# Kernel optimization log

Hardware: AMD Instinct MI355X
Metric: run time of the kernel (lower is better)

## Reference

```python
import jax, jax.numpy as jnp
import numpy as np
import math

B, N, K, H = 128, 39, 10, 256
RATIO = 0.8
K1 = math.ceil(RATIO * N)    # 32
K2 = math.ceil(RATIO * K1)   # 26
K3 = math.ceil(RATIO * K2)   # 21


def _edge_conv(x_flat, nb, n, w, b):
    # DynamicEdgeConv: per-graph kNN on features (self included, as torch_cluster.knn),
    # message = relu(Linear([x_i, x_j - x_i])), max aggregation over the K neighbors.
    f = x_flat.shape[-1]
    x = x_flat.reshape(nb, n, f)
    sq = jnp.sum(x * x, axis=-1)                                   # [nb,n]
    d = sq[:, :, None] + sq[:, None, :] - 2.0 * jnp.einsum('bif,bjf->bij', x, x)
    _, idx = jax.lax.top_k(-d, K)                                  # [nb,n,K] nearest
    xj = x[jnp.arange(nb)[:, None, None], idx]                     # [nb,n,K,f]
    xi = x[:, :, None, :]
    msg = jnp.concatenate([jnp.broadcast_to(xi, xj.shape), xj - xi], axis=-1)
    h = jax.nn.relu(msg @ w + b)
    return jnp.max(h, axis=2).reshape(nb * n, -1)


def _gcn_score(x_flat, adj, w, b):
    # GCNConv(in,1) with self-loops + symmetric normalization (SAGPool score layer)
    nb, n, _ = adj.shape
    x = x_flat.reshape(nb, n, -1)
    a = adj + jnp.eye(n, dtype=adj.dtype)
    dinv = jax.lax.rsqrt(jnp.sum(a, axis=-1))
    an = a * dinv[:, :, None] * dinv[:, None, :]
    s = jnp.einsum('bij,bjf->bif', an, x @ w) + b
    return s[..., 0]                                               # [nb,n]


def _sag_pool(x_flat, adj, k, w, b):
    # SAGPool: GCN score, per-graph top-k, gate kept nodes by tanh(score), filter adj.
    nb, n, _ = adj.shape
    score = _gcn_score(x_flat, adj, w, b)
    top, loc = jax.lax.top_k(score, k)                             # [nb,k]
    bi = jnp.arange(nb)[:, None]
    x = x_flat.reshape(nb, n, -1)
    xp = x[bi, loc] * jnp.tanh(top)[..., None]
    adj_p = adj[jnp.arange(nb)[:, None, None], loc[:, :, None], loc[:, None, :]]
    perm = (bi * n + loc).reshape(-1)                              # flat node ids
    return xp.reshape(nb * k, -1), adj_p, perm


def _bn(x, g, b, eps=1e-5):
    m = jnp.mean(x, axis=0)
    v = jnp.var(x, axis=0)
    return (x - m) * jax.lax.rsqrt(v + eps) * g + b


def _readout(x_flat, nb, k):
    x = x_flat.reshape(nb, k, -1)
    return jnp.concatenate([jnp.max(x, axis=1), jnp.mean(x, axis=1)], axis=1)


def reference(x, adj, w_mlp1, b_mlp1, w_mlp2, b_mlp2, w_mlp3, b_mlp3, w_mlp6, b_mlp6,
              bn1_g, bn1_b, bn2_g, bn2_b, bn3_g, bn3_b,
              p1_w, p1_b, p2_w, p2_b, p3_w, p3_b,
              lin1_w, lin1_b, lin2_w, lin2_b, lin3_w, lin3_b,
              lin4_w, lin4_b, lin5_w, lin5_b, lin6_w, lin6_b):
    relu = jax.nn.relu
    deg_gt = jnp.sum(adj, axis=-1).reshape(B * N)                  # degree(edge_index[0])

    def decoder(xf):
        d = jnp.tanh(_edge_conv(xf, B, N, w_mlp3, b_mlp3))         # conv4
        d = jnp.tanh(_edge_conv(d, B, N, w_mlp2, b_mlp2))          # conv5
        return _edge_conv(d, B, N, w_mlp6, b_mlp6)                 # conv6

    def degree_head(xf):
        h = relu(xf @ lin4_w + lin4_b)
        h = relu(h @ lin5_w + lin5_b)
        return relu(h @ lin6_w + lin6_b)

    # ---- level 1 ----
    h1 = relu(_bn(_edge_conv(x.reshape(B * N, N), B, N, w_mlp1, b_mlp1), bn1_g, bn1_b))
    xp1, adj1, perm1 = _sag_pool(h1, adj, K1, p1_w, p1_b)
    x_out1 = jnp.zeros_like(h1).at[perm1].set(xp1)
    x_dec1 = decoder(x_out1)
    x_degree = degree_head(x_out1)   # source reuses this tensor for levels 2/3 preds
    gt1, pred1 = deg_gt[perm1], x_degree[perm1]
    r1 = _readout(xp1, B, K1)

    # ---- level 2 ----
    h2 = relu(_bn(_edge_conv(xp1, B, K1, w_mlp2, b_mlp2), bn2_g, bn2_b))
    xp2, adj2, perm2 = _sag_pool(h2, adj1, K2, p2_w, p2_b)
    inner2 = jnp.zeros_like(h2).at[perm2].set(xp2)
    x_out2 = jnp.zeros_like(h1).at[perm1].set(inner2)
    x_dec2 = decoder(x_out2)
    gt2, pred2 = deg_gt[perm2], x_degree[perm2]
    r2 = _readout(xp2, B, K2)

    # ---- level 3 ----
    h3 = relu(_bn(_edge_conv(xp2, B, K2, w_mlp3, b_mlp3), bn3_g, bn3_b))
    xp3, adj3, perm3 = _sag_pool(h3, adj2, K3, p3_w, p3_b)
    inner3 = jnp.zeros_like(h3).at[perm3].set(xp3)
    x_out3 = jnp.zeros_like(h1).at[perm2].set(inner3)  # faithful: source uses perm_2 here
    x_dec3 = decoder(x_out3)
    gt3, pred3 = deg_gt[perm3], x_degree[perm3]
    r3 = _readout(xp3, B, K3)

    z = r1 + r2 + r3
    z = relu(z @ lin1_w + lin1_b)
    z = relu(z @ lin2_w + lin2_b)
    probs = jax.nn.softmax(z @ lin3_w + lin3_b, axis=1)
    return (probs, x_dec1, x_dec2, x_dec3, gt1, pred1, gt2, pred2, gt3, pred3)


def setup_inputs() -> dict:
    key = jax.random.key(0)
    ks = jax.random.split(key, 32)
    rn = lambda i, shape: jax.random.normal(ks[i], shape, dtype=jnp.float32) * 0.05
    x = jax.random.normal(ks[0], (B, N, N), dtype=jnp.float32)
    adj = (jax.random.uniform(ks[1], (B, N, N)) < 0.2).astype(jnp.float32)
    adj = adj * (1.0 - jnp.eye(N, dtype=jnp.float32))
    return dict(
        x=x, adj=adj,
        w_mlp1=rn(2, (2 * N, H)), b_mlp1=rn(3, (H,)),
        w_mlp2=rn(4, (2 * H, H)), b_mlp2=rn(5, (H,)),
        w_mlp3=rn(6, (2 * H, H)), b_mlp3=rn(7, (H,)),
        w_mlp6=rn(8, (2 * H, N)), b_mlp6=rn(9, (N,)),
        bn1_g=jnp.ones((H,), jnp.float32), bn1_b=jnp.zeros((H,), jnp.float32),
        bn2_g=jnp.ones((H,), jnp.float32), bn2_b=jnp.zeros((H,), jnp.float32),
        bn3_g=jnp.ones((H,), jnp.float32), bn3_b=jnp.zeros((H,), jnp.float32),
        p1_w=rn(10, (H, 1)), p1_b=rn(11, (1,)),
        p2_w=rn(12, (H, 1)), p2_b=rn(13, (1,)),
        p3_w=rn(14, (H, 1)), p3_b=rn(15, (1,)),
        lin1_w=rn(16, (2 * H, H)), lin1_b=rn(17, (H,)),
        lin2_w=rn(18, (H, H // 2)), lin2_b=rn(19, (H // 2,)),
        lin3_w=rn(20, (H // 2, 2)), lin3_b=rn(21, (2,)),
        lin4_w=rn(22, (H, H)), lin4_b=rn(23, (H,)),
        lin5_w=rn(24, (H, H // 2)), lin5_b=rn(25, (H // 2,)),
        lin6_w=rn(26, (H // 2, 1)), lin6_b=rn(27, (1,)))
```

## Files before the change

### kernel.cpp

```cpp
#include <hip/hip_runtime.h>
#include <cmath>

#define B_   128
#define N_   39
#define KNN_ 10
#define H_   256
#define K1_  32
#define K2_  26
#define K3_  21

static inline int cdiv(int a, int b) { return (a + b - 1) / b; }

typedef __attribute__((ext_vector_type(8))) short short8;
typedef __attribute__((ext_vector_type(4))) short short4v;
typedef __attribute__((ext_vector_type(4))) float floatx4;

__device__ inline short f2b(float f) {
  unsigned u = __float_as_uint(f);
  u += 0x7fff + ((u >> 16) & 1);
  return (short)(u >> 16);
}
__device__ inline float b2f(short h) {
  return __uint_as_float(((unsigned)(unsigned short)h) << 16);
}
__device__ inline void f2b3(float v, short& h, short& m, short& l) {
  h = f2b(v);
  float r1 = v - b2f(h);
  m = f2b(r1);
  l = f2b(r1 - b2f(m));
}

__device__ __forceinline__ void gl_lds16(const short* g, short* l) {
  __builtin_amdgcn_global_load_lds(
      (const __attribute__((address_space(1))) unsigned int*)g,
      (__attribute__((address_space(3))) unsigned int*)l, 16, 0, 0);
}

__global__ void prep_kernel(
    const float* __restrict__ w1, const float* __restrict__ w2,
    const float* __restrict__ w3, const float* __restrict__ w6,
    const float* __restrict__ l4, const float* __restrict__ l5,
    const float* __restrict__ x, const float* __restrict__ adj,
    short* __restrict__ wt1h, short* __restrict__ wt1m, short* __restrict__ wt1l,
    short* __restrict__ wt2h, short* __restrict__ wt2m, short* __restrict__ wt2l,
    short* __restrict__ wt3h, short* __restrict__ wt3m, short* __restrict__ wt3l,
    short* __restrict__ wt6h, short* __restrict__ wt6m,
    short* __restrict__ l4h, short* __restrict__ l4m,
    short* __restrict__ l5h, short* __restrict__ l5m,
    short* __restrict__ xsph, short* __restrict__ xspm, short* __restrict__ xspl,
    float* __restrict__ deg, short* __restrict__ zbase, double* __restrict__ bnsum) {
  int blk = blockIdx.x;
  int task, base;
  if      (blk < 128)  { task = 0; base = 0; }
  else if (blk < 640)  { task = 1; base = 128; }
  else if (blk < 1152) { task = 2; base = 640; }
  else if (blk < 1230) { task = 3; base = 1152; }
  else if (blk < 1486) { task = 4; base = 1230; }
  else if (blk < 1614) { task = 5; base = 1486; }
  else if (blk < 2862) { task = 6; base = 1614; }
  else if (blk < 2882) { task = 7; base = 2862; }
  else if (blk < 6626) { task = 8; base = 2882; }
  else                 { task = 9; base = 6626; }
  int t = (blk - base) * 256 + threadIdx.x;
  if (task == 0) {
    if (t >= 512 * 64) return;
    int nn = t >> 6, k = t & 63;
    float v = 0.f;
    if (k < 39) v = (nn < 256) ? w1[k * 256 + nn] - w1[(39 + k) * 256 + nn]
                               : w1[(39 + k) * 256 + (nn - 256)];
    short h, m, l; f2b3(v, h, m, l);
    wt1h[t] = h; wt1m[t] = m; wt1l[t] = l;
  } else if (task == 1) {
    if (t >= 512 * 256) return;
    int nn = t >> 8, k = t & 255;
    float v = (nn < 256) ? w2[k * 256 + nn] - w2[(256 + k) * 256 + nn]
                         : w2[(256 + k) * 256 + (nn - 256)];
    short h, m, l; f2b3(v, h, m, l);
    wt2h[t] = h; wt2m[t] = m; wt2l[t] = l;
  } else if (task == 2) {
    if (t >= 512 * 256) return;
    int nn = t >> 8, k = t & 255;
    float v = (nn < 256) ? w3[k * 256 + nn] - w3[(256 + k) * 256 + nn]
                         : w3[(256 + k) * 256 + (nn - 256)];
    short h, m, l; f2b3(v, h, m, l);
    wt3h[t] = h; wt3m[t] = m; wt3l[t] = l;
  } else if (task == 3) {
    if (t >= 78 * 256) return;
    int nn = t >> 8, k = t & 255;
    float v = (nn < 39) ? w6[k * 39 + nn] - w6[(256 + k) * 39 + nn]
                        : w6[(256 + k) * 39 + (nn - 39)];
    short h, m, l; f2b3(v, h, m, l);
    wt6h[t] = h; wt6m[t] = m;
  } else if (task == 4) {
    if (t >= 256 * 256) return;
    int nn = t >> 8, k = t & 255;
    short h, m, l; f2b3(l4[k * 256 + nn], h, m, l);
    l4h[t] = h; l4m[t] = m;
  } else if (task == 5) {
    if (t >= 128 * 256) return;
    int nn = t >> 8, k = t & 255;
    short h, m, l; f2b3(l5[k * 128 + nn], h, m, l);
    l5h[t] = h; l5m[t] = m;
  } else if (task == 6) {
    if (t >= 4992 * 64) return;
    int r = t >> 6, k = t & 63;
    float v = (k < 39) ? x[r * 39 + k] : 0.f;
    short h, m, l; f2b3(v, h, m, l);
    xsph[t] = h; xspm[t] = m; xspl[t] = l;
  } else if (task == 7) {
    if (t >= B_ * N_) return;
    const float* row = adj + (size_t)t * N_;
    float s = 0.f;
    for (int j = 0; j < N_; ++j) s += row[j];
    deg[t] = s;
  } else if (task == 8) {
    if (t >= 958464) return;
    short8 zz = {};
    *(short8*)&zbase[(size_t)t * 8] = zz;
  } else {
    if (t >= 256) return;
    for (int j = 0; j < 6; ++j) bnsum[t + j * 256] = 0.0;
  }
}

__global__ __launch_bounds__(512) void knn_gemm_kernel(
    const short* __restrict__ kxh, const short* __restrict__ kxm, const short* __restrict__ kxl,
    int knt, int kKs, int kn, int kF32, int* __restrict__ idx, int knnB,
    const short* __restrict__ Ah, const short* __restrict__ Am, const short* __restrict__ Al,
    int gnt, int gK,
    const short* __restrict__ Wh, const short* __restrict__ Wm, const short* __restrict__ Wl,
    float* __restrict__ C0, int gM, int gN, int gyB,
    size_t Astride, size_t Cstride) {
  extern __shared__ char smem[];
  int tid = threadIdx.x;
  int wave = tid >> 6, lane = tid & 63;
  int lm = lane & 15, lk = (lane >> 4) * 8;
  if ((int)blockIdx.x < knnB) {
    short* sh_h = (short*)smem;
    short* sh_m = sh_h + 48 * 40;
    short* sh_l = sh_m + 48 * 40;
    float* Gs   = (float*)(sh_l + 48 * 40);
    float* diag = Gs + 48 * 49;
    int b = blockIdx.x;
    int nt = (kn + 15) >> 4;
    int tasks = nt * nt;
    floatx4 acc[2] = {};
    int stage_elems = 384 * knt;
    for (int k0 = 0; k0 < kF32; k0 += 32) {
      for (int e = tid; e < stage_elems; e += 512) {
        int a = e / 384, rem = e - a * 384;
        int r = rem >> 3, c4 = (rem & 7) * 4;
        const short* src = (a == 0) ? kxh : (a == 1) ? kxm : kxl;
        short* dst = (a == 0) ? sh_h : (a == 1) ? sh_m : sh_l;
        *(short4v*)&dst[r * 40 + c4] =
            *(const short4v*)&src[((size_t)(b * kn + r)) * kKs + k0 + c4];
      }
      __syncthreads();
#pragma unroll
      for (int ai = 0; ai < 2; ++ai) {
        int t = wave + ai * 8;
        if (t < tasks) {
          int ti = t / nt, tj = t - ti * nt;
          int ra = (ti * 16 + lm) * 40 + lk;
          int rb = (tj * 16 + lm) * 40 + lk;
          short8 ah = *(const short8*)&sh_h[ra];
          short8 am = *(const short8*)&sh_m[ra];
          short8 bh = *(const short8*)&sh_h[rb];
          short8 bm = *(const short8*)&sh_m[rb];
          floatx4 a = acc[ai];
          a = __builtin_amdgcn_mfma_f32_16x16x32_bf16(ah, bh, a, 0, 0, 0);
          a = __builtin_amdgcn_mfma_f32_16x16x32_bf16(ah, bm, a, 0, 0, 0);
          a = __builtin_amdgcn_mfma_f32_16x16x32_bf16(am, bh, a, 0, 0, 0);
          if (knt == 3) {
            short8 al = *(const short8*)&sh_l[ra];
            short8 bl = *(const short8*)&sh_l[rb];
            a = __builtin_amdgcn_mfma_f32_16x16x32_bf16(ah, bl, a, 0, 0, 0);
            a = __builtin_amdgcn_mfma_f32_16x16x32_bf16(al, bh, a, 0, 0, 0);
            a = __builtin_amdgcn_mfma_f32_16x16x32_bf16(am, bm, a, 0, 0, 0);
          }
          acc[ai] = a;
        }
      }
      __syncthreads();
    }
#pragma unroll
    for (int ai = 0; ai < 2; ++ai) {
      int t = wave + ai * 8;
      if (t < tasks) {
        int ti = t / nt, tj = t - ti * nt;
        int col = tj * 16 + lm;
        int rbase = ti * 16 + (lane >> 4) * 4;
#pragma unroll
        for (int r = 0; r < 4; ++r) Gs[(rbase + r) * 49 + col] = acc[ai][r];
      }
    }
    __syncthreads();
    if (tid < 48) diag[tid] = (tid < kn) ? Gs[tid * 49 + tid] : INFINITY;
    __syncthreads();
    for (int row = wave; row < kn; row += 8) {
      float gii = diag[row];
      float dj = (lane < kn) ? (gii + diag[lane] - 2.f * Gs[row * 49 + lane]) : INFINITY;
      int rank = 0;
      for (int j = 0; j < kn; ++j) {
        float djp = gii + diag[j] - 2.f * Gs[row * 49 + j];
        rank += (djp < dj || (djp == dj && j < lane)) ? 1 : 0;
      }
      if (lane < kn && rank < KNN_)
        idx[(size_t)(b * kn + row) * KNN_ + rank] = lane;
    }
  } else {
    short* AshL = (short*)smem;
    short* AsmL = AshL + 4096;
    short* AslL = AsmL + 4096;
    short* BshL = (short*)smem + gnt * 4096;
    short* BsmL = BshL + 4096;
    short* BslL = BsmL + 4096;
    int gb = blockIdx.x - knnB;
    int gxB = (gN + 127) >> 7;
    int nb = (int)gridDim.x - knnB;
    int xcd = gb & 7, j = gb >> 3;
    int q8 = nb >> 3, r8 = nb & 7;
    int work = (xcd < r8 ? xcd * (q8 + 1) : r8 * (q8 + 1) + (xcd - r8) * q8) + j;
    int gx = work % gxB;
    int rest = work / gxB;
    int gy = rest % gyB;
    int gz = rest / gyB;
    const short* A_h = Ah + (size_t)gz * Astride;
    const short* A_m = Am ? Am + (size_t)gz * Astride : nullptr;
    const short* A_l = Al ? Al + (size_t)gz * Astride : nullptr;
    float* C = C0 + (size_t)gz * Cstride;
    int row0 = gy * 128, col0 = gx * 128;
    int wm = wave & 1, wn = wave >> 1;
    int srow = tid >> 2;
    int scs = ((tid & 3) ^ ((srow >> 1) & 3)) << 3;
    size_t gArow = (size_t)(row0 + srow) * gK;
    size_t gBrow = (size_t)(col0 + srow) * gK;
    short* ldsA = AshL + tid * 8;
    short* ldsAm = AsmL + tid * 8;
    short* ldsAl = AslL + tid * 8;
    short* ldsB = BshL + tid * 8;
    short* ldsBm = BsmL + tid * 8;
    short* ldsBl = BslL + tid * 8;
    floatx4 acc[4][2] = {};
    for (int k0 = 0; k0 < gK; k0 += 32) {
      gl_lds16(A_h + gArow + k0 + scs, ldsA);
      gl_lds16(A_m + gArow + k0 + scs, ldsAm);
      if (gnt == 3) gl_lds16(A_l + gArow + k0 + scs, ldsAl);
      gl_lds16(Wh + gBrow + k0 + scs, ldsB);
      gl_lds16(Wm + gBrow + k0 + scs, ldsBm);
      if (gnt == 3) gl_lds16(Wl + gBrow + k0 + scs, ldsBl);
      __syncthreads();
      short8 afh[4], afm[4], afl[4];
#pragma unroll
      for (int mi = 0; mi < 4; ++mi) {
        int rr = wm * 64 + mi * 16 + lm;
        int ro = rr * 32 + (((lane >> 4) ^ ((rr >> 1) & 3)) << 3);
        afh[mi] = *(const short8*)&AshL[ro];
        afm[mi] = *(const short8*)&AsmL[ro];
        if (gnt == 3) afl[mi] = *(const short8*)&AslL[ro];
      }
#pragma unroll
      for (int ni = 0; ni < 2; ++ni) {
        int rb = wn * 32 + ni * 16 + lm;
        int ro = rb * 32 + (((lane >> 4) ^ ((rb >> 1) & 3)) << 3);
        short8 bfh = *(const short8*)&BshL[ro];
        short8 bfm = *(const short8*)&BsmL[ro];
#pragma unroll
        for (int mi = 0; mi < 4; ++mi) {
          floatx4 a = acc[mi][ni];
          a = __builtin_amdgcn_mfma_f32_16x16x32_bf16(afh[mi], bfh, a, 0, 0, 0);
          a = __builtin_amdgcn_mfma_f32_16x16x32_bf16(afh[mi], bfm, a, 0, 0, 0);
          a = __builtin_amdgcn_mfma_f32_16x16x32_bf16(afm[mi], bfh, a, 0, 0, 0);
          if (gnt == 3) {
            short8 bfl = *(const short8*)&BslL[ro];
            a = __builtin_amdgcn_mfma_f32_16x16x32_bf16(afh[mi], bfl, a, 0, 0, 0);
            a = __builtin_amdgcn_mfma_f32_16x16x32_bf16(afl[mi], bfh, a, 0, 0, 0);
            a = __builtin_amdgcn_mfma_f32_16x16x32_bf16(afm[mi], bfm, a, 0, 0, 0);
          }
          acc[mi][ni] = a;
        }
      }
      __syncthreads();
    }
    int lr = (lane >> 4) * 4;
#pragma unroll
    for (int mi = 0; mi < 4; ++mi)
#pragma unroll
      for (int ni = 0; ni < 2; ++ni) {
        int colg = col0 + wn * 32 + ni * 16 + lm;
        if (colg >= gN) continue;
#pragma unroll
        for (int r = 0; r < 4; ++r) {
          int rowg = row0 + wm * 64 + mi * 16 + lr + r;
          C[(size_t)rowg * gN + colg] = acc[mi][ni][r];
        }
      }
  }
}

__global__ __launch_bounds__(256) void degree_head_kernel(
    const short* __restrict__ Xh, const short* __restrict__ Xm,
    const short* __restrict__ W4h, const short* __restrict__ W4m, const float* __restrict__ b4,
    const short* __restrict__ W5h, const short* __restrict__ W5m, const float* __restrict__ b5,
    const float* __restrict__ w6, const float* __restrict__ b6,
    float* __restrict__ xdeg) {
  __shared__ __attribute__((aligned(16))) short Ash[32 * 40];
  __shared__ __attribute__((aligned(16))) short Asm[32 * 40];
  __shared__ __attribute__((aligned(16))) short Bsh[256 * 40];
  __shared__ __attribute__((aligned(16))) short Bsm[256 * 40];
  __shared__ __attribute__((aligned(16))) short H1h[32][264];
  __shared__ __attribute__((aligned(16))) short H1m[32][264];
  __shared__ float rowsum[32];
  int tid = threadIdx.x;
  int wave = tid >> 6, lane = tid & 63;
  int lm = lane & 15, g = lane >> 4, lk = g * 8;
  int row0 = blockIdx.x * 32;

  floatx4 acc[2][4] = {};
  for (int k0 = 0; k0 < 256; k0 += 32) {
    {
      int e = tid;
      int a = e >> 7, rem = e & 127;
      int r = rem >> 2, kc = (rem & 3) * 8;
      const short* src = a ? Xm : Xh;
      short* dst = a ? Asm : Ash;
      *(short8*)&dst[r * 40 + kc] = *(const short8*)&src[(size_t)(row0 + r) * 256 + k0 + kc];
    }
#pragma unroll
    for (int i = 0; i < 8; ++i) {
      int e = tid + i * 256;
      int a = e >> 10, rem = e & 1023;
      int r = rem >> 2, kc = (rem & 3) * 8;
      const short* src = a ? W4m : W4h;
      short* dst = a ? Bsm : Bsh;
      *(short8*)&dst[r * 40 + kc] = *(const short8*)&src[(size_t)r * 256 + k0 + kc];
    }
    __syncthreads();
    short8 afh[2], afm[2];
#pragma unroll
    for (int rt = 0; rt < 2; ++rt) {
      int ro = (rt * 16 + lm) * 40 + lk;
      afh[rt] = *(const short8*)&Ash[ro];
      afm[rt] = *(const short8*)&Asm[ro];
    }
#pragma unroll
    for (int ct = 0; ct < 4; ++ct) {
      int ro = (wave * 64 + ct * 16 + lm) * 40 + lk;
      short8 bfh = *(const short8*)&Bsh[ro];
      short8 bfm = *(const short8*)&Bsm[ro];
#pragma unroll
      for (int rt = 0; rt < 2; ++rt) {
        floatx4 a = acc[rt][ct];
        a = __builtin_amdgcn_mfma_f32_16x16x32_bf16(afh[rt], bfh, a, 0, 0, 0);
        a = __builtin_amdgcn_mfma_f32_16x16x32_bf16(afh[rt], bfm, a, 0, 0, 0);
        a = __builtin_amdgcn_mfma_f32_16x16x32_bf16(afm[rt], bfh, a, 0, 0, 0);
        acc[rt][ct] = a;
      }
    }
    __syncthreads();
  }
#pragma unroll
  for (int rt = 0; rt < 2; ++rt)
#pragma unroll
    for (int ct = 0; ct < 4; ++ct) {
      int col = wave * 64 + ct * 16 + lm;
      float bv = b4[col];
#pragma unroll
      for (int r = 0; r < 4; ++r) {
        int row = rt * 16 + g * 4 + r;
        float v = fmaxf(acc[rt][ct][r] + bv, 0.f);
        short hh = f2b(v);
        H1h[row][col] = hh;
        H1m[row][col] = f2b(v - b2f(hh));
      }
    }
  if (tid < 32) rowsum[tid] = 0.f;
  __syncthreads();

  floatx4 acc2[2][2] = {};
  for (int k0 = 0; k0 < 256; k0 += 32) {
#pragma unroll
    for (int i = 0; i < 4; ++i) {
      int e = tid + i * 256;
      int a = e >> 9, rem = e & 511;
      int r = rem >> 2, kc = (rem & 3) * 8;
      const short* src = a ? W5m : W5h;
      short* dst = a ? Bsm : Bsh;
      *(short8*)&dst[r * 40 + kc] = *(const short8*)&src[(size_t)r * 256 + k0 + kc];
    }
    __syncthreads();
    short8 afh[2], afm[2];
#pragma unroll
    for (int rt = 0; rt < 2; ++rt) {
      afh[rt] = *(const short8*)&H1h[rt * 16 + lm][k0 + lk];
      afm[rt] = *(const short8*)&H1m[rt * 16 + lm][k0 + lk];
    }
#pragma unroll
    for (int ct = 0; ct < 2; ++ct) {
      int ro = (wave * 32 + ct * 16 + lm) * 40 + lk;
      short8 bfh = *(const short8*)&Bsh[ro];
      short8 bfm = *(const short8*)&Bsm[ro];
#pragma unroll
      for (int rt = 0; rt < 2; ++rt) {
        floatx4 a = acc2[rt][ct];
        a = __builtin_amdgcn_mfma_f32_16x16x32_bf16(afh[rt], bfh, a, 0, 0, 0);
        a = __builtin_amdgcn_mfma_f32_16x16x32_bf16(afh[rt], bfm, a, 0, 0, 0);
        a = __builtin_amdgcn_mfma_f32_16x16x32_bf16(afm[rt], bfh, a, 0, 0, 0);
        acc2[rt][ct] = a;
      }
    }
    __syncthreads();
  }
#pragma unroll
  for (int rt = 0; rt < 2; ++rt) {
#pragma unroll
    for (int r = 0; r < 4; ++r) {
      float p = 0.f;
#pragma unroll
      for (int ct = 0; ct < 2; ++ct) {
        int col = wave * 32 + ct * 16 + lm;
        float v = fmaxf(acc2[rt][ct][r] + b5[col], 0.f);
        p += v * w6[col];
      }
#pragma unroll
      for (int off = 1; off < 16; off <<= 1) p += __shfl_xor(p, off, 64);
      if (lm == 0) atomicAdd(&rowsum[rt * 16 + g * 4 + r], p);
    }
  }
  __syncthreads();
  if (tid < 32) xdeg[row0 + tid] = fmaxf(rowsum[tid] + b6[0], 0.f);
}

__global__ void edge_agg_kernel(const float* __restrict__ AB, const float* __restrict__ bias,
                                const int* __restrict__ idx, int n, int Hc, int act,
                                int rows, int per,
                                float* __restrict__ out,
                                short* __restrict__ outh, short* __restrict__ outm,
                                short* __restrict__ outl) {
  int t = blockIdx.x * blockDim.x + threadIdx.x;
  if (t >= rows * Hc) return;
  int r = t / Hc, h = t - r * Hc;
  int d = r / per, rloc = r - d * per;
  int b = rloc / n;
  int s2 = 2 * Hc;
  float av = AB[(size_t)r * s2 + h] + bias[h];
  const int* ir = idx + ((size_t)d * per + rloc) * KNN_;
  int base = d * per + b * n;
  float m = -INFINITY;
  for (int k = 0; k < KNN_; ++k) {
    float v = av + AB[(size_t)(base + ir[k]) * s2 + Hc + h];
    v = fmaxf(v, 0.f);
    m = fmaxf(m, v);
  }
  if (act == 2) m = tanhf(m);
  if (out) out[t] = m;
  if (outh) {
    short hh, mm, ll;
    f2b3(m, hh, mm, ll);
    outh[t] = hh; outm[t] = mm;
    if (outl) outl[t] = ll;
  }
}

__global__ __launch_bounds__(256) void edge_agg4_kernel(
    const float* __restrict__ AB, const float* __restrict__ bias,
    const int* __restrict__ idx, int n, int Hc, int act,
    int rows, int per,
    float* __restrict__ out,
    short* __restrict__ outh, short* __restrict__ outm, short* __restrict__ outl,
    double* __restrict__ colsums) {
  __shared__ double lds_s[4][256];
  __shared__ double lds_s2[4][256];
  int tid = threadIdx.x;
  int hq = tid & 63, rl = tid >> 6;
  int h = hq << 2;
  int s2s = 2 * Hc;
  double cs[4] = {0.0, 0.0, 0.0, 0.0}, cs2[4] = {0.0, 0.0, 0.0, 0.0};
#pragma unroll
  for (int sub = 0; sub < 2; ++sub) {
    int r = blockIdx.x * 8 + rl + sub * 4;
    if (r < rows) {
      int d = r / per, rloc = r - d * per;
      int b = rloc / n;
      float4 av = *(const float4*)&AB[(size_t)r * s2s + h];
      float4 bv = *(const float4*)&bias[h];
      float a0 = av.x + bv.x, a1 = av.y + bv.y, a2 = av.z + bv.z, a3 = av.w + bv.w;
      const int* ir = idx + ((size_t)d * per + rloc) * KNN_;
      int base = d * per + b * n;
      int nb[KNN_];
#pragma unroll
      for (int k = 0; k < KNN_; ++k) nb[k] = base + ir[k];
      float m0 = -INFINITY, m1 = -INFINITY, m2 = -INFINITY, m3 = -INFINITY;
#pragma unroll
      for (int k = 0; k < KNN_; ++k) {
        float4 bb = *(const float4*)&AB[(size_t)nb[k] * s2s + Hc + h];
        m0 = fmaxf(m0, fmaxf(a0 + bb.x, 0.f));
        m1 = fmaxf(m1, fmaxf(a1 + bb.y, 0.f));
        m2 = fmaxf(m2, fmaxf(a2 + bb.z, 0.f));
        m3 = fmaxf(m3, fmaxf(a3 + bb.w, 0.f));
      }
      if (act == 2) { m0 = tanhf(m0); m1 = tanhf(m1); m2 = tanhf(m2); m3 = tanhf(m3); }
      size_t o = (size_t)r * Hc + h;
      if (out) *(float4*)&out[o] = make_float4(m0, m1, m2, m3);
      if (outh) {
        short h0, mm0, l0, h1, mm1, l1, h2, mm2, l2, h3, mm3, l3;
        f2b3(m0, h0, mm0, l0); f2b3(m1, h1, mm1, l1);
        f2b3(m2, h2, mm2, l2); f2b3(m3, h3, mm3, l3);
        short4v vh = {h0, h1, h2, h3};
        short4v vm = {mm0, mm1, mm2, mm3};
        *(short4v*)&outh[o] = vh;
        *(short4v*)&outm[o] = vm;
        if (outl) {
          short4v vl = {l0, l1, l2, l3};
          *(short4v*)&outl[o] = vl;
        }
      }
      if (colsums) {
        double d0 = (double)m0, d1 = (double)m1, d2 = (double)m2, d3 = (double)m3;
        cs[0] += d0; cs2[0] += d0 * d0;
        cs[1] += d1; cs2[1] += d1 * d1;
        cs[2] += d2; cs2[2] += d2 * d2;
        cs[3] += d3; cs2[3] += d3 * d3;
      }
    }
  }
  if (colsums) {
#pragma unroll
    for (int j = 0; j < 4; ++j) {
      lds_s[rl][h + j] = cs[j];
      lds_s2[rl][h + j] = cs2[j];
    }
    __syncthreads();
    int c = tid;
    double ss = ((lds_s[0][c] + lds_s[1][c]) + lds_s[2][c]) + lds_s[3][c];
    double ss2 = ((lds_s2[0][c] + lds_s2[1][c]) + lds_s2[2][c]) + lds_s2[3][c];
    atomicAdd(&colsums[c], ss);
    atomicAdd(&colsums[256 + c], ss2);
  }
}

__global__ __launch_bounds__(1024) void sag_pool_kernel(
    const float* __restrict__ t1,
    const double* __restrict__ colsums, const float* __restrict__ bng,
    const float* __restrict__ bnb, int M,
    const float* __restrict__ pw,
    const float* __restrict__ adj_in, int n, int k,
    const float* __restrict__ pb,
    int* __restrict__ perm, float* __restrict__ adjp,
    const float* __restrict__ deg, const float* __restrict__ xdeg,
    float* __restrict__ gt, float* __restrict__ pred,
    const int* __restrict__ gperm, int gk, float* __restrict__ ggt, float* __restrict__ gpred,
    const int* __restrict__ remap, int accum,
    short* __restrict__ xph, short* __restrict__ xpm, short* __restrict__ xpl,
    short* __restrict__ soh, short* __restrict__ som, float* __restrict__ z,
    const float* __restrict__ W1, const float* __restrict__ b1,
    const float* __restrict__ W2, const float* __restrict__ b2,
    const float* __restrict__ W3, const float* __restrict__ b3,
    float* __restrict__ probs) {
  __shared__ float ys[40], dinv[40], scs[40], tant[40];
  __shared__ int locs[40];
  __shared__ __attribute__((aligned(16))) float t1L[39 * 256];
  __shared__ __attribute__((aligned(16))) float adjL[39 * 39];
  __shared__ __attribute__((aligned(16))) float scshL[512];
  __shared__ __attribute__((aligned(16))) float pmx[4][256];
  __shared__ __attribute__((aligned(16))) float psm[4][256];
  __shared__ __attribute__((aligned(16))) float ca[512];
  __shared__ __attribute__((aligned(16))) float z1s[256];
  __shared__ __attribute__((aligned(16))) float z2s[128];
  __shared__ float lg[2];
  int b = blockIdx.x;
  int i = threadIdx.x;
  int wave = i >> 6, lane = i & 63;
  {
    const float* src = t1 + (size_t)(b * n) * H_;
    int tot = n * H_;
    for (int e = i; e < tot; e += 1024) t1L[e] = src[e];
    const float* asrc = adj_in + (size_t)b * n * n;
    int atot = n * n;
    for (int e = i; e < atot; e += 1024) adjL[e] = asrc[e];
  }
  if (i < 256) {
    double mean = colsums[i] / M;
    double var = colsums[256 + i] / M - mean * mean;
    float rstd = 1.f / sqrtf((float)var + 1e-5f);
    float sc = rstd * bng[i];
    scshL[i] = sc;
    scshL[256 + i] = bnb[i] - (float)mean * sc;
  }
  __syncthreads();
  for (int row = wave; row < n; row += 16) {
    const float* xr = &t1L[row * H_];
    float s = 0.f;
    for (int kk = lane; kk < H_; kk += 64) {
      float v = fmaxf(xr[kk] * scshL[kk] + scshL[H_ + kk], 0.f);
      s += v * pw[kk];
    }
    for (int off = 32; off; off >>= 1) s += __shfl_down(s, off, 64);
    if (lane == 0) ys[row] = s;
  }
  __syncthreads();
  if (i < n) {
    const float* ar = &adjL[i * n];
    float sum = 1.f;
    for (int j = 0; j < n; ++j) sum += ar[j];
    dinv[i] = 1.f / sqrtf(sum);
  }
  __syncthreads();
  if (i < n) {
    const float* ar = &adjL[i * n];
    float acc = 0.f;
    for (int j = 0; j < n; ++j) {
      float a = ar[j] + (i == j ? 1.f : 0.f);
      acc += a * dinv[j] * ys[j];
    }
    scs[i] = dinv[i] * acc + pb[0];
  }
  __syncthreads();
  if (i < n) {
    float si = scs[i];
    int rank = 0;
    for (int j = 0; j < n; ++j) {
      float sj = scs[j];
      rank += (sj > si || (sj == si && j < i)) ? 1 : 0;
    }
    if (rank < k) {
      tant[rank] = tanhf(si);
      locs[rank] = i;
      perm[b * k + rank] = b * n + i;
    }
  }
  __syncthreads();
  if (adjp) {
    for (int e = threadIdx.x; e < k * k; e += 1024) {
      int t1i = e / k, t2i = e - t1i * k;
      adjp[(size_t)b * k * k + e] = adjL[locs[t1i] * n + locs[t2i]];
    }
  }
  if (gt && threadIdx.x < k) {
    int p = b * n + locs[threadIdx.x];
    gt[b * k + threadIdx.x] = deg[p];
    pred[b * k + threadIdx.x] = xdeg[p];
  }
  if (ggt && threadIdx.x < gk) {
    int p = gperm[b * gk + threadIdx.x];
    ggt[b * gk + threadIdx.x] = deg[p];
    gpred[b * gk + threadIdx.x] = xdeg[p];
  }
  int hc = i & 255;
  int rg = i >> 8;
  float sc = scshL[hc], sh = scshL[H_ + hc];
  float mx = -INFINITY, sm = 0.f;
  for (int r = rg; r < k; r += 4) {
    int loc = locs[r];
    float tg = tant[r];
    float v = fmaxf(t1L[loc * H_ + hc] * sc + sh, 0.f) * tg;
    short hh, mm, ll;
    f2b3(v, hh, mm, ll);
    size_t xo = ((size_t)(b * k + r)) * H_ + hc;
    xph[xo] = hh; xpm[xo] = mm; xpl[xo] = ll;
    int own = b * n + loc;
    int tgt = remap ? remap[own] : own;
    size_t so = (size_t)tgt * H_ + hc;
    soh[so] = hh; som[so] = mm;
    float vq = b2f(hh) + b2f(mm) + b2f(ll);
    mx = fmaxf(mx, vq);
    sm += vq;
  }
  pmx[rg][hc] = mx;
  psm[rg][hc] = sm;
  __syncthreads();
  if (i < 256) {
    float m0 = fmaxf(fmaxf(pmx[0][hc], pmx[1][hc]), fmaxf(pmx[2][hc], pmx[3][hc]));
    float s0 = ((psm[0][hc] + psm[1][hc]) + psm[2][hc]) + psm[3][hc];
    float* zb = z + (size_t)b * 2 * H_;
    float mean = s0 / (float)k;
    float zr1, zr2;
    if (accum) { zr1 = zb[hc] + m0; zr2 = zb[H_ + hc] + mean; zb[hc] = zr1; zb[H_ + hc] = zr2; }
    else       { zr1 = m0;  zr2 = mean; zb[hc] = zr1; zb[H_ + hc] = zr2; }
    if (probs) { ca[hc] = zr1; ca[H_ + hc] = zr2; }
  }
  if (probs) {
    __syncthreads();
    if (i < 256) {
      int c = hc;
      float s = 0.f;
      for (int kk = 0; kk < 512; kk += 4) {
        float4 av = *(const float4*)&ca[kk];
        s += av.x * W1[(size_t)kk * 256 + c];
        s += av.y * W1[(size_t)(kk + 1) * 256 + c];
        s += av.z * W1[(size_t)(kk + 2) * 256 + c];
        s += av.w * W1[(size_t)(kk + 3) * 256 + c];
      }
      z1s[c] = fmaxf(s + b1[c], 0.f);
    }
    __syncthreads();
    if (i < 128) {
      int c = i;
      float s = 0.f;
      for (int kk = 0; kk < 256; kk += 4) {
        float4 av = *(const float4*)&z1s[kk];
        s += av.x * W2[(size_t)kk * 128 + c];
        s += av.y * W2[(size_t)(kk + 1) * 128 + c];
        s += av.z * W2[(size_t)(kk + 2) * 128 + c];
        s += av.w * W2[(size_t)(kk + 3) * 128 + c];
      }
      z2s[c] = fmaxf(s + b2[c], 0.f);
    }
    __syncthreads();
    if (wave < 2) {
      float s = 0.f;
      for (int kk = lane; kk < 128; kk += 64) s += z2s[kk] * W3[(size_t)kk * 2 + wave];
      for (int off = 32; off; off >>= 1) s += __shfl_down(s, off, 64);
      if (lane == 0) lg[wave] = s + b3[wave];
    }
    __syncthreads();
    if (i == 0) {
      float aa = lg[0], cc = lg[1];
      float m = fmaxf(aa, cc);
      float ea = expf(aa - m), ec = expf(cc - m);
      float inv = 1.f / (ea + ec);
      probs[2 * b] = ea * inv;
      probs[2 * b + 1] = ec * inv;
    }
  }
}

extern "C" void kernel_launch(void* const* d_in, const int* in_sizes, int n_in,
                              void* d_out, int out_size, void* d_ws, size_t ws_size,
                              hipStream_t stream) {
  auto in = [&](int i) { return (const float*)d_in[i]; };
  const float* x      = in(0);
  const float* adj    = in(1);
  const float* w_mlp1 = in(2);  const float* b_mlp1 = in(3);
  const float* w_mlp2 = in(4);  const float* b_mlp2 = in(5);
  const float* w_mlp3 = in(6);  const float* b_mlp3 = in(7);
  const float* w_mlp6 = in(8);  const float* b_mlp6 = in(9);
  const float* bn1_g = in(10);  const float* bn1_b = in(11);
  const float* bn2_g = in(12);  const float* bn2_b = in(13);
  const float* bn3_g = in(14);  const float* bn3_b = in(15);
  const float* p1_w = in(16);   const float* p1_b = in(17);
  const float* p2_w = in(18);   const float* p2_b = in(19);
  const float* p3_w = in(20);   const float* p3_b = in(21);
  const float* lin1_w = in(22); const float* lin1_b = in(23);
  const float* lin2_w = in(24); const float* lin2_b = in(25);
  const float* lin3_w = in(26); const float* lin3_b = in(27);
  const float* lin4_w = in(28); const float* lin4_b = in(29);
  const float* lin5_w = in(30); const float* lin5_b = in(31);
  const float* lin6_w = in(32); const float* lin6_b = in(33);

  float* out = (float*)d_out;
  float* out_probs = out;
  float* out_dec1  = out_probs + 256;
  float* out_gt1   = out_dec1 + 3 * 4992 * 39;
  float* out_pred1 = out_gt1 + 4096;
  float* out_gt2   = out_pred1 + 4096;
  float* out_pred2 = out_gt2 + 3328;
  float* out_gt3   = out_pred2 + 3328;
  float* out_pred3 = out_gt3 + 2688;

  char* base = (char*)d_ws;
  size_t off = 0;
  auto allocf = [&](size_t n) -> float* {
    float* p = (float*)(base + off);
    off += ((n * sizeof(float) + 255) & ~(size_t)255);
    return p;
  };
  auto alloci = [&](size_t n) -> int* {
    int* p = (int*)(base + off);
    off += ((n * sizeof(int) + 255) & ~(size_t)255);
    return p;
  };
  auto allocs = [&](size_t n) -> short* {
    short* p = (short*)(base + off);
    off += ((n * sizeof(short) + 255) & ~(size_t)255);
    return p;
  };
  auto allocd = [&](size_t n) -> double* {
    double* p = (double*)(base + off);
    off += ((n * sizeof(double) + 255) & ~(size_t)255);
    return p;
  };

  const size_t S = (size_t)4992 * 256;
  const size_t AB_S = (size_t)4992 * 512;
  const int SI = 4992 * KNN_;

  short* wt1h = allocs(512 * 64); short* wt1m = allocs(512 * 64); short* wt1l = allocs(512 * 64);
  short* wt2h = allocs(512 * 256); short* wt2m = allocs(512 * 256); short* wt2l = allocs(512 * 256);
  short* wt3h = allocs(512 * 256); short* wt3m = allocs(512 * 256); short* wt3l = allocs(512 * 256);
  short* wt6h = allocs(78 * 256);  short* wt6m = allocs(78 * 256);
  short* l4h = allocs(256 * 256);  short* l4m = allocs(256 * 256);
  short* l5h = allocs(128 * 256);  short* l5m = allocs(128 * 256);
  short* xsph = allocs(4992 * 64); short* xspm = allocs(4992 * 64); short* xspl = allocs(4992 * 64);
  float* deg  = allocf(4992);
  float* xdeg = allocf(4992);
  int* idxb = alloci(3 * SI);
  float* AB3 = allocf(3 * AB_S);
  float* trunk_t1 = allocf(S);
  double* bnsum = allocd(3 * 512);
  short* xph = allocs((size_t)4096 * 256); short* xpm = allocs((size_t)4096 * 256); short* xpl = allocs((size_t)4096 * 256);
  short* xoutb_h = allocs(3 * S);
  short* xoutb_m = allocs(3 * S);
  short* t1b_h = allocs(3 * S);
  short* t1b_m = allocs(3 * S);
  float* adj1 = allocf(128 * 32 * 32);
  float* adj2 = allocf(128 * 26 * 26);
  int* perm1 = alloci(4096); int* perm2 = alloci(3328); int* perm3 = alloci(2688);
  float* z  = allocf(128 * 512);
  if (off > ws_size) return;

  short* t2b_h = xoutb_h; short* t2b_m = xoutb_m;

  const size_t LDS3 = 6 * 128 * 32 * sizeof(short);
  const size_t LDS2 = 4 * 128 * 32 * sizeof(short);

  prep_kernel<<<6627, 256, 0, stream>>>(
      w_mlp1, w_mlp2, w_mlp3, w_mlp6, lin4_w, lin5_w, x, adj,
      wt1h, wt1m, wt1l, wt2h, wt2m, wt2l, wt3h, wt3m, wt3l, wt6h, wt6m,
      l4h, l4m, l5h, l5m, xsph, xspm, xspl, deg, xoutb_h, bnsum);

  knn_gemm_kernel<<<B_ + 4 * 39, 512, LDS3, stream>>>(
      xsph, xspm, xspl, 3, 64, N_, 64, idxb, B_,
      xsph, xspm, xspl, 3, 64, wt1h, wt1m, wt1l, AB3, 4992, 512, 39, 0, 0);
  edge_agg4_kernel<<<4992 / 8, 256, 0, stream>>>(AB3, b_mlp1, idxb, N_, 256, 0, 4992, 4992,
                                                 trunk_t1, nullptr, nullptr, nullptr, bnsum);
  sag_pool_kernel<<<B_, 1024, 0, stream>>>(
      trunk_t1, bnsum, bn1_g, bn1_b, 4992, p1_w, adj, N_, K1_, p1_b,
      perm1, adj1, nullptr, nullptr, nullptr, nullptr,
      nullptr, 0, nullptr, nullptr,
      nullptr, 0, xph, xpm, xpl, xoutb_h, xoutb_m, z,
      nullptr, nullptr, nullptr, nullptr, nullptr, nullptr, nullptr);
  degree_head_kernel<<<156, 256, 0, stream>>>(
      xoutb_h, xoutb_m, l4h, l4m, lin4_b, l5h, l5m, lin5_b, lin6_w, lin6_b, xdeg);

  knn_gemm_kernel<<<B_ + 4 * 32, 512, LDS3, stream>>>(
      xph, xpm, xpl, 3, 256, K1_, 256, idxb, B_,
      xph, xpm, xpl, 3, 256, wt2h, wt2m, wt2l, AB3, 4096, 512, 32, 0, 0);
  edge_agg4_kernel<<<4096 / 8, 256, 0, stream>>>(AB3, b_mlp2, idxb, K1_, 256, 0, 4096, 4096,
                                                 trunk_t1, nullptr, nullptr, nullptr, bnsum + 512);
  sag_pool_kernel<<<B_, 1024, 0, stream>>>(
      trunk_t1, bnsum + 512, bn2_g, bn2_b, 4096, p2_w, adj1, K1_, K2_, p2_b,
      perm2, adj2, deg, xdeg, out_gt2, out_pred2,
      perm1, K1_, out_gt1, out_pred1,
      perm1, 1, xph, xpm, xpl, xoutb_h + S, xoutb_m + S, z,
      nullptr, nullptr, nullptr, nullptr, nullptr, nullptr, nullptr);

  knn_gemm_kernel<<<B_ + 4 * 26, 512, LDS3, stream>>>(
      xph, xpm, xpl, 3, 256, K2_, 256, idxb, B_,
      xph, xpm, xpl, 3, 256, wt3h, wt3m, wt3l, AB3, 3328, 512, 26, 0, 0);
  edge_agg4_kernel<<<3328 / 8, 256, 0, stream>>>(AB3, b_mlp3, idxb, K2_, 256, 0, 3328, 3328,
                                                 trunk_t1, nullptr, nullptr, nullptr, bnsum + 1024);
  sag_pool_kernel<<<B_, 1024, 0, stream>>>(
      trunk_t1, bnsum + 1024, bn3_g, bn3_b, 3328, p3_w, adj2, K2_, K3_, p3_b,
      perm3, nullptr, deg, xdeg, out_gt3, out_pred3,
      nullptr, 0, nullptr, nullptr,
      perm2, 1, xph, xpm, xpl, xoutb_h + 2 * S, xoutb_m + 2 * S, z,
      lin1_w, lin1_b, lin2_w, lin2_b, lin3_w, lin3_b, out_probs);

  knn_gemm_kernel<<<3 * B_ + 4 * 39 * 3, 512, LDS2, stream>>>(
      xoutb_h, xoutb_m, nullptr, 2, 256, N_, 256, idxb, 3 * B_,
      xoutb_h, xoutb_m, nullptr, 2, 256, wt3h, wt3m, nullptr, AB3, 4992, 512, 39, S, AB_S);
  edge_agg4_kernel<<<3 * 4992 / 8, 256, 0, stream>>>(
      AB3, b_mlp3, idxb, N_, 256, 2, 3 * 4992, 4992, nullptr, t1b_h, t1b_m, nullptr, nullptr);
  knn_gemm_kernel<<<3 * B_ + 4 * 39 * 3, 512, LDS2, stream>>>(
      t1b_h, t1b_m, nullptr, 2, 256, N_, 256, idxb, 3 * B_,
      t1b_h, t1b_m, nullptr, 2, 256, wt2h, wt2m, nullptr, AB3, 4992, 512, 39, S, AB_S);
  edge_agg4_kernel<<<3 * 4992 / 8, 256, 0, stream>>>(
      AB3, b_mlp2, idxb, N_, 256, 2, 3 * 4992, 4992, nullptr, t2b_h, t2b_m, nullptr, nullptr);
  knn_gemm_kernel<<<3 * B_ + 1 * 39 * 3, 512, LDS2, stream>>>(
      t2b_h, t2b_m, nullptr, 2, 256, N_, 256, idxb, 3 * B_,
      t2b_h, t2b_m, nullptr, 2, 256, wt6h, wt6m, nullptr, AB3, 4992, 78, 39, S, (size_t)4992 * 78);
  edge_agg_kernel<<<cdiv(3 * 4992 * 39, 256), 256, 0, stream>>>(
      AB3, b_mlp6, idxb, N_, 39, 0, 3 * 4992, 4992, out_dec1, nullptr, nullptr, nullptr);
}
```

Before: 428.1 us.

## Fuse decoder kNN/GEMM/aggregation stages into one cooperative persistent kernel

Replaces six decoder kernel launches (three kNN+GEMM and three edge-aggregation passes) with a single cooperative kernel of 512 blocks. Block roles are distributed in loops and grid.sync() separates the stages. The aim is to remove launch overhead and inter-kernel gaps on a small, latency-bound workload. In exchange, grid-wide barriers add their own cost, and the fixed grid may leave some CUs underused. The old launch sequence is kept as a fallback for when the cooperative launch fails or occupancy is too low.

```diff
diff --git a/kernel.cpp b/kernel.cpp
--- a/kernel.cpp
+++ b/kernel.cpp
@@ -1,5 +1,8 @@
 #include <hip/hip_runtime.h>
+#include <hip/hip_cooperative_groups.h>
 #include <cmath>
+
+namespace cg = cooperative_groups;
 
 #define B_   128
 #define N_   39
@@ -298,6 +301,256 @@
   }
 }
 
+__device__ __forceinline__ void dec_knn_block(char* smem, int b,
+    const short* __restrict__ kxh, const short* __restrict__ kxm, int* __restrict__ idx) {
+  int tid = threadIdx.x;
+  int wave = tid >> 6, lane = tid & 63;
+  int lm = lane & 15, lk = (lane >> 4) * 8;
+  short* sh_h = (short*)smem;
+  short* sh_m = sh_h + 48 * 40;
+  short* sh_l = sh_m + 48 * 40;
+  float* Gs   = (float*)(sh_l + 48 * 40);
+  float* diag = Gs + 48 * 49;
+  const int kn = 39, kKs = 256, kF32 = 256, nt = 3, tasks = 9;
+  floatx4 acc[2] = {};
+  for (int k0 = 0; k0 < kF32; k0 += 32) {
+    for (int e = tid; e < 768; e += 512) {
+      int a = e / 384, rem = e - a * 384;
+      int r = rem >> 3, c4 = (rem & 7) * 4;
+      const short* src = (a == 0) ? kxh : kxm;
+      short* dst = (a == 0) ? sh_h : sh_m;
+      *(short4v*)&dst[r * 40 + c4] =
+          *(const short4v*)&src[((size_t)(b * kn + r)) * kKs + k0 + c4];
+    }
+    __syncthreads();
+#pragma unroll
+    for (int ai = 0; ai < 2; ++ai) {
+      int t = wave + ai * 8;
+      if (t < tasks) {
+        int ti = t / nt, tj = t - ti * nt;
+        int ra = (ti * 16 + lm) * 40 + lk;
+        int rb = (tj * 16 + lm) * 40 + lk;
+        short8 ah = *(const short8*)&sh_h[ra];
+        short8 am = *(const short8*)&sh_m[ra];
+        short8 bh = *(const short8*)&sh_h[rb];
+        short8 bm = *(const short8*)&sh_m[rb];
+        floatx4 a = acc[ai];
+        a = __builtin_amdgcn_mfma_f32_16x16x32_bf16(ah, bh, a, 0, 0, 0);
+        a = __builtin_amdgcn_mfma_f32_16x16x32_bf16(ah, bm, a, 0, 0, 0);
+        a = __builtin_amdgcn_mfma_f32_16x16x32_bf16(am, bh, a, 0, 0, 0);
+        acc[ai] = a;
+      }
+    }
+    __syncthreads();
+  }
+#pragma unroll
+  for (int ai = 0; ai < 2; ++ai) {
+    int t = wave + ai * 8;
+    if (t < tasks) {
+      int ti = t / nt, tj = t - ti * nt;
+      int col = tj * 16 + lm;
+      int rbase = ti * 16 + (lane >> 4) * 4;
+#pragma unroll
+      for (int r = 0; r < 4; ++r) Gs[(rbase + r) * 49 + col] = acc[ai][r];
+    }
+  }
+  __syncthreads();
+  if (tid < 48) diag[tid] = (tid < kn) ? Gs[tid * 49 + tid] : INFINITY;
+  __syncthreads();
+  for (int row = wave; row < kn; row += 8) {
+    float gii = diag[row];
+    float dj = (lane < kn) ? (gii + diag[lane] - 2.f * Gs[row * 49 + lane]) : INFINITY;
+    int rank = 0;
+    for (int j = 0; j < kn; ++j) {
+      float djp = gii + diag[j] - 2.f * Gs[row * 49 + j];
+      rank += (djp < dj || (djp == dj && j < lane)) ? 1 : 0;
+    }
+    if (lane < kn && rank < KNN_)
+      idx[(size_t)(b * kn + row) * KNN_ + rank] = lane;
+  }
+  __syncthreads();
+}
+
+__device__ __forceinline__ void dec_gemm_block(char* smem, int gb, int nb,
+    const short* __restrict__ Ah, const short* __restrict__ Am,
+    const short* __restrict__ Wh, const short* __restrict__ Wm,
+    float* __restrict__ C0, int gN, size_t Astride, size_t Cstride) {
+  int tid = threadIdx.x;
+  int wave = tid >> 6, lane = tid & 63;
+  int lm = lane & 15;
+  short* AshL = (short*)smem;
+  short* AsmL = AshL + 4096;
+  short* BshL = AsmL + 4096;
+  short* BsmL = BshL + 4096;
+  const int gK = 256, gyB = 39;
+  int gxB = (gN + 127) >> 7;
+  int xcd = gb & 7, j = gb >> 3;
+  int q8 = nb >> 3, r8 = nb & 7;
+  int work = (xcd < r8 ? xcd * (q8 + 1) : r8 * (q8 + 1) + (xcd - r8) * q8) + j;
+  int gx = work % gxB;
+  int rest = work / gxB;
+  int gy = rest % gyB;
+  int gz = rest / gyB;
+  const short* A_h = Ah + (size_t)gz * Astride;
+  const short* A_m = Am + (size_t)gz * Astride;
+  float* C = C0 + (size_t)gz * Cstride;
+  int row0 = gy * 128, col0 = gx * 128;
+  int wm = wave & 1, wn = wave >> 1;
+  int srow = tid >> 2;
+  int scs = ((tid & 3) ^ ((srow >> 1) & 3)) << 3;
+  size_t gArow = (size_t)(row0 + srow) * gK;
+  size_t gBrow = (size_t)(col0 + srow) * gK;
+  short* ldsA = AshL + tid * 8;
+  short* ldsAm = AsmL + tid * 8;
+  short* ldsB = BshL + tid * 8;
+  short* ldsBm = BsmL + tid * 8;
+  floatx4 acc[4][2] = {};
+  for (int k0 = 0; k0 < gK; k0 += 32) {
+    gl_lds16(A_h + gArow + k0 + scs, ldsA);
+    gl_lds16(A_m + gArow + k0 + scs, ldsAm);
+    gl_lds16(Wh + gBrow + k0 + scs, ldsB);
+    gl_lds16(Wm + gBrow + k0 + scs, ldsBm);
+    __syncthreads();
+    short8 afh[4], afm[4];
+#pragma unroll
+    for (int mi = 0; mi < 4; ++mi) {
+      int rr = wm * 64 + mi * 16 + lm;
+      int ro = rr * 32 + (((lane >> 4) ^ ((rr >> 1) & 3)) << 3);
+      afh[mi] = *(const short8*)&AshL[ro];
+      afm[mi] = *(const short8*)&AsmL[ro];
+    }
+#pragma unroll
+    for (int ni = 0; ni < 2; ++ni) {
+      int rb = wn * 32 + ni * 16 + lm;
+      int ro = rb * 32 + (((lane >> 4) ^ ((rb >> 1) & 3)) << 3);
+      short8 bfh = *(const short8*)&BshL[ro];
+      short8 bfm = *(const short8*)&BsmL[ro];
+#pragma unroll
+      for (int mi = 0; mi < 4; ++mi) {
+        floatx4 a = acc[mi][ni];
+        a = __builtin_amdgcn_mfma_f32_16x16x32_bf16(afh[mi], bfh, a, 0, 0, 0);
+        a = __builtin_amdgcn_mfma_f32_16x16x32_bf16(afh[mi], bfm, a, 0, 0, 0);
+        a = __builtin_amdgcn_mfma_f32_16x16x32_bf16(afm[mi], bfh, a, 0, 0, 0);
+        acc[mi][ni] = a;
+      }
+    }
+    __syncthreads();
+  }
+  int lr = (lane >> 4) * 4;
+#pragma unroll
+  for (int mi = 0; mi < 4; ++mi)
+#pragma unroll
+    for (int ni = 0; ni < 2; ++ni) {
+      int colg = col0 + wn * 32 + ni * 16 + lm;
+      if (colg >= gN) continue;
+#pragma unroll
+      for (int r = 0; r < 4; ++r) {
+        int rowg = row0 + wm * 64 + mi * 16 + lr + r;
+        C[(size_t)rowg * gN + colg] = acc[mi][ni][r];
+      }
+    }
+}
+
+__device__ __forceinline__ void dec_agg4_grid(int gid0, int gsize,
+    const float* __restrict__ AB, const float* __restrict__ bias,
+    const int* __restrict__ idx,
+    short* __restrict__ outh, short* __restrict__ outm) {
+  const int rows = 14976, per = 4992, n = 39, Hc = 256, s2s = 512;
+  int total = rows * 64;
+  for (int u = gid0; u < total; u += gsize) {
+    int r = u >> 6, hq = u & 63;
+    int h = hq << 2;
+    int d = r / per, rloc = r - d * per;
+    int b = rloc / n;
+    float4 av = *(const float4*)&AB[(size_t)r * s2s + h];
+    float4 bv = *(const float4*)&bias[h];
+    float a0 = av.x + bv.x, a1 = av.y + bv.y, a2 = av.z + bv.z, a3 = av.w + bv.w;
+    const int* ir = idx + ((size_t)d * per + rloc) * KNN_;
+    int base = d * per + b * n;
+    int nb[KNN_];
+#pragma unroll
+    for (int k = 0; k < KNN_; ++k) nb[k] = base + ir[k];
+    float m0 = -INFINITY, m1 = -INFINITY, m2 = -INFINITY, m3 = -INFINITY;
+#pragma unroll
+    for (int k = 0; k < KNN_; ++k) {
+      float4 bb = *(const float4*)&AB[(size_t)nb[k] * s2s + Hc + h];
+      m0 = fmaxf(m0, fmaxf(a0 + bb.x, 0.f));
+      m1 = fmaxf(m1, fmaxf(a1 + bb.y, 0.f));
+      m2 = fmaxf(m2, fmaxf(a2 + bb.z, 0.f));
+      m3 = fmaxf(m3, fmaxf(a3 + bb.w, 0.f));
+    }
+    m0 = tanhf(m0); m1 = tanhf(m1); m2 = tanhf(m2); m3 = tanhf(m3);
+    size_t o = (size_t)r * Hc + h;
+    short h0, mm0, l0, h1, mm1, l1, h2, mm2, l2, h3, mm3, l3;
+    f2b3(m0, h0, mm0, l0); f2b3(m1, h1, mm1, l1);
+    f2b3(m2, h2, mm2, l2); f2b3(m3, h3, mm3, l3);
+    short4v vh = {h0, h1, h2, h3};
+    short4v vm = {mm0, mm1, mm2, mm3};
+    *(short4v*)&outh[o] = vh;
+    *(short4v*)&outm[o] = vm;
+  }
+}
+
+__device__ __forceinline__ void dec_aggs_grid(int gid0, int gsize,
+    const float* __restrict__ AB, const float* __restrict__ bias,
+    const int* __restrict__ idx, float* __restrict__ out) {
+  const int rows = 14976, per = 4992, n = 39, Hc = 39, s2 = 78;
+  int total = rows * Hc;
+  for (int t = gid0; t < total; t += gsize) {
+    int r = t / Hc, h = t - r * Hc;
+    int d = r / per, rloc = r - d * per;
+    int b = rloc / n;
+    float av = AB[(size_t)r * s2 + h] + bias[h];
+    const int* ir = idx + ((size_t)d * per + rloc) * KNN_;
+    int base = d * per + b * n;
+    float m = -INFINITY;
+    for (int k = 0; k < KNN_; ++k) {
+      float v = av + AB[(size_t)(base + ir[k]) * s2 + Hc + h];
+      v = fmaxf(v, 0.f);
+      m = fmaxf(m, v);
+    }
+    out[t] = m;
+  }
+}
+
+struct DecP {
+  const short *xoh, *xom, *wt3h, *wt3m, *wt2h, *wt2m, *wt6h, *wt6m;
+  const float *b3, *b2, *b6;
+  short *t1h, *t1m, *t2h, *t2m;
+  float *AB3, *outdec;
+  int *idxb;
+  size_t S, ABS, C3S;
+};
+
+__global__ __launch_bounds__(512) void dec_coop_kernel(DecP p) {
+  extern __shared__ char smem[];
+  cg::grid_group grid = cg::this_grid();
+  int bid = blockIdx.x;
+  int nbk = (int)gridDim.x;
+  int gid0 = bid * 512 + threadIdx.x;
+  int gsize = nbk * 512;
+  for (int role = bid; role < 852; role += nbk) {
+    if (role < 384) dec_knn_block(smem, role, p.xoh, p.xom, p.idxb);
+    else dec_gemm_block(smem, role - 384, 468, p.xoh, p.xom, p.wt3h, p.wt3m, p.AB3, 512, p.S, p.ABS);
+  }
+  grid.sync();
+  dec_agg4_grid(gid0, gsize, p.AB3, p.b3, p.idxb, p.t1h, p.t1m);
+  grid.sync();
+  for (int role = bid; role < 852; role += nbk) {
+    if (role < 384) dec_knn_block(smem, role, p.t1h, p.t1m, p.idxb);
+    else dec_gemm_block(smem, role - 384, 468, p.t1h, p.t1m, p.wt2h, p.wt2m, p.AB3, 512, p.S, p.ABS);
+  }
+  grid.sync();
+  dec_agg4_grid(gid0, gsize, p.AB3, p.b2, p.idxb, p.t2h, p.t2m);
+  grid.sync();
+  for (int role = bid; role < 501; role += nbk) {
+    if (role < 384) dec_knn_block(smem, role, p.t2h, p.t2m, p.idxb);
+    else dec_gemm_block(smem, role - 384, 117, p.t2h, p.t2m, p.wt6h, p.wt6m, p.AB3, 78, p.S, p.C3S);
+  }
+  grid.sync();
+  dec_aggs_grid(gid0, gsize, p.AB3, p.b6, p.idxb, p.outdec);
+}
+
 __global__ __launch_bounds__(256) void degree_head_kernel(
     const short* __restrict__ Xh, const short* __restrict__ Xm,
     const short* __restrict__ W4h, const short* __restrict__ W4m, const float* __restrict__ b4,
@@ -857,19 +1110,43 @@
       perm2, 1, xph, xpm, xpl, xoutb_h + 2 * S, xoutb_m + 2 * S, z,
       lin1_w, lin1_b, lin2_w, lin2_b, lin3_w, lin3_b, out_probs);
 
-  knn_gemm_kernel<<<3 * B_ + 4 * 39 * 3, 512, LDS2, stream>>>(
-      xoutb_h, xoutb_m, nullptr, 2, 256, N_, 256, idxb, 3 * B_,
-      xoutb_h, xoutb_m, nullptr, 2, 256, wt3h, wt3m, nullptr, AB3, 4992, 512, 39, S, AB_S);
-  edge_agg4_kernel<<<3 * 4992 / 8, 256, 0, stream>>>(
-      AB3, b_mlp3, idxb, N_, 256, 2, 3 * 4992, 4992, nullptr, t1b_h, t1b_m, nullptr, nullptr);
-  knn_gemm_kernel<<<3 * B_ + 4 * 39 * 3, 512, LDS2, stream>>>(
-      t1b_h, t1b_m, nullptr, 2, 256, N_, 256, idxb, 3 * B_,
-      t1b_h, t1b_m, nullptr, 2, 256, wt2h, wt2m, nullptr, AB3, 4992, 512, 39, S, AB_S);
-  edge_agg4_kernel<<<3 * 4992 / 8, 256, 0, stream>>>(
-      AB3, b_mlp2, idxb, N_, 256, 2, 3 * 4992, 4992, nullptr, t2b_h, t2b_m, nullptr, nullptr);
-  knn_gemm_kernel<<<3 * B_ + 1 * 39 * 3, 512, LDS2, stream>>>(
-      t2b_h, t2b_m, nullptr, 2, 256, N_, 256, idxb, 3 * B_,
-      t2b_h, t2b_m, nullptr, 2, 256, wt6h, wt6m, nullptr, AB3, 4992, 78, 39, S, (size_t)4992 * 78);
-  edge_agg_kernel<<<cdiv(3 * 4992 * 39, 256), 256, 0, stream>>>(
-      AB3, b_mlp6, idxb, N_, 39, 0, 3 * 4992, 4992, out_dec1, nullptr, nullptr, nullptr);
-}
+  DecP p;
+  p.xoh = xoutb_h; p.xom = xoutb_m;
+  p.wt3h = wt3h; p.wt3m = wt3m;
+  p.wt2h = wt2h; p.wt2m = wt2m;
+  p.wt6h = wt6h; p.wt6m = wt6m;
+  p.b3 = b_mlp3; p.b2 = b_mlp2; p.b6 = b_mlp6;
+  p.t1h = t1b_h; p.t1m = t1b_m;
+  p.t2h = t2b_h; p.t2m = t2b_m;
+  p.AB3 = AB3; p.outdec = out_dec1;
+  p.idxb = idxb;
+  p.S = S; p.ABS = AB_S; p.C3S = (size_t)4992 * 78;
+
+  int maxB = 0;
+  bool coop =
+      (hipOccupancyMaxActiveBlocksPerMultiprocessor(&maxB, dec_coop_kernel, 512, LDS2)
+           == hipSuccess) && maxB >= 2;
+  if (coop) {
+    void* kargs[] = { (void*)&p };
+    coop = hipLaunchCooperativeKernel(reinterpret_cast<const void*>(dec_coop_kernel),
+                                      dim3(512), dim3(512), kargs, (unsigned)LDS2,
+                                      stream) == hipSuccess;
+  }
+  if (!coop) {
+    knn_gemm_kernel<<<3 * B_ + 4 * 39 * 3, 512, LDS2, stream>>>(
+        xoutb_h, xoutb_m, nullptr, 2, 256, N_, 256, idxb, 3 * B_,
+        xoutb_h, xoutb_m, nullptr, 2, 256, wt3h, wt3m, nullptr, AB3, 4992, 512, 39, S, AB_S);
+    edge_agg4_kernel<<<3 * 4992 / 8, 256, 0, stream>>>(
+        AB3, b_mlp3, idxb, N_, 256, 2, 3 * 4992, 4992, nullptr, t1b_h, t1b_m, nullptr, nullptr);
+    knn_gemm_kernel<<<3 * B_ + 4 * 39 * 3, 512, LDS2, stream>>>(
+        t1b_h, t1b_m, nullptr, 2, 256, N_, 256, idxb, 3 * B_,
+        t1b_h, t1b_m, nullptr, 2, 256, wt2h, wt2m, nullptr, AB3, 4992, 512, 39, S, AB_S);
+    edge_agg4_kernel<<<3 * 4992 / 8, 256, 0, stream>>>(
+        AB3, b_mlp2, idxb, N_, 256, 2, 3 * 4992, 4992, nullptr, t2b_h, t2b_m, nullptr, nullptr);
+    knn_gemm_kernel<<<3 * B_ + 1 * 39 * 3, 512, LDS2, stream>>>(
+        t2b_h, t2b_m, nullptr, 2, 256, N_, 256, idxb, 3 * B_,
+        t2b_h, t2b_m, nullptr, 2, 256, wt6h, wt6m, nullptr, AB3, 4992, 78, 39, S, (size_t)4992 * 78);
+    edge_agg_kernel<<<cdiv(3 * 4992 * 39, 256), 256, 0, stream>>>(
+        AB3, b_mlp6, idxb, N_, 39, 0, 3 * 4992, 4992, out_dec1, nullptr, nullptr, nullptr);
+  }
+}
```

Result: no change. 427.5 us (-0.1%).
